# Performance work log

Hardware: AMD Instinct MI355X
Metric: run time of the kernel (lower is better)

The kernel has to match this reference:

```python
import jax, jax.numpy as jnp
import numpy as np

B, S, D = 1, 4096, 512
H, DK, DV = 8, 64, 64


def setup_inputs() -> dict:
    key = jax.random.key(0)
    ks = jax.random.split(key, 8)
    s = 1.0 / np.sqrt(D)
    return {
        "queries": jax.random.normal(ks[0], (B, S, D), jnp.float32),
        "keys": jax.random.normal(ks[1], (B, S, D), jnp.float32),
        "values": jax.random.normal(ks[2], (B, S, D), jnp.float32),
        # Linear weights stored as [in, out] for x @ W
        "Wq": jax.random.normal(ks[3], (D, H * DK), jnp.float32) * s,
        "Wk": jax.random.normal(ks[4], (D, H * DK), jnp.float32) * s,
        "Wv": jax.random.normal(ks[5], (D, H * DV), jnp.float32) * s,
        "Wo": jax.random.normal(ks[6], (H * DV, D), jnp.float32) * s,
        "bo": jax.random.normal(ks[7], (D,), jnp.float32) * 0.02,
    }


def reference(queries, keys, values, Wq, Wk, Wv, Wo, bo):
    b, qlen = values.shape[0], queries.shape[1]
    q = (queries @ Wq).reshape(b, qlen, H, DK)
    k = (keys @ Wk).reshape(b, keys.shape[1], H, DK)
    v = (values @ Wv).reshape(b, values.shape[1], H, DV)
    scale = DK ** 0.5
    # naive full attention: materialize [b, h, sq, sk] scores
    scores = jnp.einsum("bqhd,bkhd->bhqk", q, k) / scale
    attn = jax.nn.softmax(scores, axis=-1)
    out = jnp.einsum("bhqk,bkhd->bqhd", attn, v).reshape(b, qlen, H * DV)
    out = out @ Wo + bo          # first fc_out
    out = out @ Wo + bo          # second fc_out (module applies it twice when not reversible)
    return out
```

## Files before the change

### kernel.cpp

```cpp
#include <hip/hip_runtime.h>

#define S_LEN  4096
#define DMODEL 512
#define NH     8
#define HD     64

typedef _Float16 f16x8 __attribute__((ext_vector_type(8)));
typedef _Float16 f16x4 __attribute__((ext_vector_type(4)));
typedef float    f32x4 __attribute__((ext_vector_type(4)));

static __device__ __forceinline__ unsigned short f2h(float x) {
  return __builtin_bit_cast(unsigned short, (_Float16)x);
}

__global__ __launch_bounds__(256) void wtrans_kernel(
    const float* __restrict__ w0, const float* __restrict__ w1,
    const float* __restrict__ w2, const float* __restrict__ w3,
    unsigned short* __restrict__ o0, unsigned short* __restrict__ o1,
    unsigned short* __restrict__ o2, unsigned short* __restrict__ o3,
    unsigned short* __restrict__ o3s)
{
  __shared__ unsigned short T[64 * 72];
  const float* W; unsigned short* O;
  switch (blockIdx.z) {
    case 0:  W = w0; O = o0; break;
    case 1:  W = w1; O = o1; break;
    case 2:  W = w2; O = o2; break;
    default: W = w3; O = o3; break;
  }
  const int tid = threadIdx.x;
  const int k0 = blockIdx.x * 64, n0 = blockIdx.y * 64;
  const int c4 = (tid & 15) * 4;
#pragma unroll
  for (int rp = 0; rp < 4; ++rp) {
    int r = rp * 16 + (tid >> 4);
    float4 x = *(const float4*)(W + (k0 + r) * DMODEL + n0 + c4);
    T[(c4 + 0) * 72 + r] = f2h(x.x);
    T[(c4 + 1) * 72 + r] = f2h(x.y);
    T[(c4 + 2) * 72 + r] = f2h(x.z);
    T[(c4 + 3) * 72 + r] = f2h(x.w);
    if (blockIdx.z == 3) {
      f16x4 st;
      st[0] = (_Float16)x.x; st[1] = (_Float16)x.y;
      st[2] = (_Float16)x.z; st[3] = (_Float16)x.w;
      *(f16x4*)&o3s[(k0 + r) * DMODEL + n0 + c4] = st;
    }
  }
  __syncthreads();
#pragma unroll
  for (int it = 0; it < 2; ++it) {
    int i = tid + it * 256;
    int nl = i >> 3, c = i & 7;
    *(f16x8*)&O[(n0 + nl) * DMODEL + k0 + c * 8] = *(const f16x8*)&T[nl * 72 + c * 8];
  }
}

__global__ __launch_bounds__(256) void gemm128_kernel(
    const void* __restrict__ A0, const void* __restrict__ A1,
    const void* __restrict__ A2, const void* __restrict__ A3,
    const unsigned short* __restrict__ B0, const unsigned short* __restrict__ B1,
    const unsigned short* __restrict__ B2, const unsigned short* __restrict__ B3,
    void* __restrict__ C0, void* __restrict__ C1,
    void* __restrict__ C2, void* __restrict__ C3,
    const float* __restrict__ bias, unsigned short* __restrict__ vtg,
    const float* __restrict__ wo_f32, const float* __restrict__ bo_in,
    float* __restrict__ bo2_out,
    int a_fp32_mask, int c_fp32_mask)
{
  constexpr int K = DMODEL, N = DMODEL;
  __shared__ unsigned short As[128 * 32];
  __shared__ unsigned short Bs[128 * 32];
  const int z = blockIdx.z;
  if (z == 3 && blockIdx.x >= 4) {
    if (blockIdx.x < 12 && blockIdx.y == 0 && wo_f32) {
      int col = (blockIdx.x - 4) * 64 + (threadIdx.x & 63);
      float s = bo_in[col];
#pragma unroll 8
      for (int j = 0; j < DMODEL; ++j) s = fmaf(bo_in[j], wo_f32[j * DMODEL + col], s);
      bo2_out[col] = s;
    }
    return;
  }
  const void* Av; const unsigned short* Bt; void* Cv;
  switch (z) {
    case 0:  Av = A0; Bt = B0; Cv = C0; break;
    case 1:  Av = A1; Bt = B1; Cv = C1; break;
    case 2:  Av = A2; Bt = B2; Cv = C2; break;
    default: Av = A3; Bt = B3; Cv = C3; break;
  }
  const int a_fp32 = (a_fp32_mask >> z) & 1;
  const int c_fp32 = (c_fp32_mask >> z) & 1;
  const int tid  = threadIdx.x;
  const int lane = tid & 63;
  const int wid  = tid >> 6;
  const int quad = lane >> 4, l16 = lane & 15;
  const int m0 = blockIdx.x * 128, n0 = blockIdx.y * 128;
  const int wm = (wid >> 1) * 64, wn = (wid & 1) * 64;
  f32x4 acc[4][4] = {};

  f16x8 areg[2], breg[2];
#pragma unroll
  for (int it = 0; it < 2; ++it) {
    int s = it * 256 + tid;
    int r = s >> 2, ck = (s & 3) * 8;
    if (a_fp32) {
      const float* p = (const float*)Av + (m0 + r) * K + ck;
      float4 x = *(const float4*)p;
      float4 y = *(const float4*)(p + 4);
      f16x8 av;
      av[0] = (_Float16)x.x; av[1] = (_Float16)x.y;
      av[2] = (_Float16)x.z; av[3] = (_Float16)x.w;
      av[4] = (_Float16)y.x; av[5] = (_Float16)y.y;
      av[6] = (_Float16)y.z; av[7] = (_Float16)y.w;
      areg[it] = av;
    } else {
      areg[it] = *(const f16x8*)((const unsigned short*)Av + (m0 + r) * K + ck);
    }
    breg[it] = *(const f16x8*)(Bt + (n0 + r) * K + ck);
  }

  for (int k0 = 0; k0 < K; k0 += 32) {
    __syncthreads();
#pragma unroll
    for (int it = 0; it < 2; ++it) {
      int s = it * 256 + tid;
      int r = s >> 2, ck = (s & 3) * 8;
      *(f16x8*)&As[r * 32 + ck] = areg[it];
      *(f16x8*)&Bs[r * 32 + ck] = breg[it];
    }
    __syncthreads();

    if (k0 + 32 < K) {
      int kk = k0 + 32;
#pragma unroll
      for (int it = 0; it < 2; ++it) {
        int s = it * 256 + tid;
        int r = s >> 2, ck = (s & 3) * 8;
        if (a_fp32) {
          const float* p = (const float*)Av + (m0 + r) * K + kk + ck;
          float4 x = *(const float4*)p;
          float4 y = *(const float4*)(p + 4);
          f16x8 av;
          av[0] = (_Float16)x.x; av[1] = (_Float16)x.y;
          av[2] = (_Float16)x.z; av[3] = (_Float16)x.w;
          av[4] = (_Float16)y.x; av[5] = (_Float16)y.y;
          av[6] = (_Float16)y.z; av[7] = (_Float16)y.w;
          areg[it] = av;
        } else {
          areg[it] = *(const f16x8*)((const unsigned short*)Av + (m0 + r) * K + kk + ck);
        }
        breg[it] = *(const f16x8*)(Bt + (n0 + r) * K + kk + ck);
      }
    }

    f16x8 af[4], bf[4];
#pragma unroll
    for (int mt = 0; mt < 4; ++mt)
      af[mt] = *(const f16x8*)&As[(wm + mt * 16 + l16) * 32 + quad * 8];
#pragma unroll
    for (int nt = 0; nt < 4; ++nt)
      bf[nt] = *(const f16x8*)&Bs[(wn + nt * 16 + l16) * 32 + quad * 8];
#pragma unroll
    for (int mt = 0; mt < 4; ++mt)
#pragma unroll
      for (int nt = 0; nt < 4; ++nt)
        acc[mt][nt] = __builtin_amdgcn_mfma_f32_16x16x32_f16(af[mt], bf[nt], acc[mt][nt], 0, 0, 0);
  }

  const int do_vt = (vtg != nullptr) && (z == 2);
#pragma unroll
  for (int mt = 0; mt < 4; ++mt)
#pragma unroll
    for (int nt = 0; nt < 4; ++nt) {
      int col = n0 + wn + nt * 16 + l16;
      float bv = bias ? bias[col] : 0.f;
#pragma unroll
      for (int g = 0; g < 4; ++g) {
        int row = m0 + wm + mt * 16 + quad * 4 + g;
        float val = acc[mt][nt][g] + bv;
        if (do_vt)        vtg[col * S_LEN + row] = f2h(val);
        else if (c_fp32)  ((float*)Cv)[row * N + col] = val;
        else              ((unsigned short*)Cv)[row * N + col] = f2h(val);
      }
    }
}

__global__ __launch_bounds__(256) void attn_kernel(
    const unsigned short* __restrict__ Qb, const unsigned short* __restrict__ Kb,
    const unsigned short* __restrict__ VtG,
    float* __restrict__ P0, unsigned short* __restrict__ P1,
    float* __restrict__ mp, float* __restrict__ lp)
{
  __shared__ unsigned short Ks[2][64 * 72];
  __shared__ unsigned short Vt[2 * 64 * 64];
  __shared__ float Msc[2][2][16];
  __shared__ float Lsc[2][2][16];

  const int tid  = threadIdx.x;
  const int lane = tid & 63;
  const int wid  = tid >> 6;
  const int qp   = wid & 1;
  const int kh   = wid >> 1;
  const int quad = lane >> 4, l16 = lane & 15;
  const int qb = blockIdx.x, h = blockIdx.y, z = blockIdx.z;
  const int hc = h * HD;
  const int qbase = qb * 64 + qp * 32;
  const int kz = z * 2048;

  f16x8 bq[2][2];
#pragma unroll
  for (int s = 0; s < 2; ++s) {
    int qrow = qbase + s * 16 + l16;
    bq[s][0] = *(const f16x8*)(Qb + qrow * DMODEL + hc + quad * 8);
    bq[s][1] = *(const f16x8*)(Qb + qrow * DMODEL + hc + 32 + quad * 8);
  }

  f32x4 o[2][4] = {};
  float m_run[2] = {-1e30f, -1e30f}, l_run[2] = {0.f, 0.f};

  f16x8 kreg[4], vreg[4];
#pragma unroll
  for (int it = 0; it < 4; ++it) {
    int s = it * 256 + tid;
    int khs = s >> 9, n = (s >> 3) & 63, c = s & 7;
    kreg[it] = *(const f16x8*)(Kb + (kz + khs * 1024 + n) * DMODEL + hc + c * 8);
    vreg[it] = *(const f16x8*)(VtG + (hc + n) * S_LEN + kz + khs * 1024 + c * 8);
  }

  for (int kbi = 0; kbi < 16; ++kbi) {
    __syncthreads();
#pragma unroll
    for (int it = 0; it < 4; ++it) {
      int s = it * 256 + tid;
      int khs = s >> 9, n = (s >> 3) & 63, c = s & 7;
      *(f16x8*)&Ks[khs][n * 72 + c * 8] = kreg[it];
      int vbase = (khs * 64 + n) * 16;
      int n15 = n & 15;
      f16x4 lo = __builtin_shufflevector(vreg[it], vreg[it], 0, 1, 2, 3);
      f16x4 hi = __builtin_shufflevector(vreg[it], vreg[it], 4, 5, 6, 7);
      *(f16x4*)&Vt[(vbase + ((2 * c) ^ n15)) * 4]     = lo;
      *(f16x4*)&Vt[(vbase + ((2 * c + 1) ^ n15)) * 4] = hi;
    }
    __syncthreads();

    if (kbi + 1 < 16) {
      int kb1 = (kbi + 1) * 64;
#pragma unroll
      for (int it = 0; it < 4; ++it) {
        int s = it * 256 + tid;
        int khs = s >> 9, n = (s >> 3) & 63, c = s & 7;
        kreg[it] = *(const f16x8*)(Kb + (kz + khs * 1024 + kb1 + n) * DMODEL + hc + c * 8);
        vreg[it] = *(const f16x8*)(VtG + (hc + n) * S_LEN + kz + khs * 1024 + kb1 + c * 8);
      }
    }

    f32x4 sT[2][4];
#pragma unroll
    for (int kt = 0; kt < 4; ++kt) {
      f16x8 ak0 = *(const f16x8*)&Ks[kh][(kt * 16 + l16) * 72 + quad * 8];
      f16x8 ak1 = *(const f16x8*)&Ks[kh][(kt * 16 + l16) * 72 + 32 + quad * 8];
#pragma unroll
      for (int s = 0; s < 2; ++s) {
        f32x4 a = {};
        a = __builtin_amdgcn_mfma_f32_16x16x32_f16(ak0, bq[s][0], a, 0, 0, 0);
        a = __builtin_amdgcn_mfma_f32_16x16x32_f16(ak1, bq[s][1], a, 0, 0, 0);
        sT[s][kt] = a;
      }
    }

    f16x4 pa[2][4];
#pragma unroll
    for (int s = 0; s < 2; ++s) {
      float vmax = -1e30f;
#pragma unroll
      for (int kt = 0; kt < 4; ++kt)
#pragma unroll
        for (int g = 0; g < 4; ++g) vmax = fmaxf(vmax, sT[s][kt][g]);
      vmax = fmaxf(vmax, __shfl_xor(vmax, 16));
      vmax = fmaxf(vmax, __shfl_xor(vmax, 32));

      if (__all(vmax <= m_run[s] + 8.0f)) {
        const float mn = m_run[s];
        float rs = 0.f;
#pragma unroll
        for (int kt = 0; kt < 4; ++kt)
#pragma unroll
          for (int g = 0; g < 4; ++g) {
            float p = __expf((sT[s][kt][g] - mn) * 0.125f);
            rs += p;
            pa[s][kt][g] = (_Float16)p;
          }
        rs += __shfl_xor(rs, 16);
        rs += __shfl_xor(rs, 32);
        l_run[s] += rs;
      } else {
        const float mn = fmaxf(m_run[s], vmax);
        const float alpha = __expf((m_run[s] - mn) * 0.125f);
        m_run[s] = mn;

        float rs = 0.f;
#pragma unroll
        for (int kt = 0; kt < 4; ++kt)
#pragma unroll
          for (int g = 0; g < 4; ++g) {
            float p = __expf((sT[s][kt][g] - mn) * 0.125f);
            rs += p;
            pa[s][kt][g] = (_Float16)p;
          }
        rs += __shfl_xor(rs, 16);
        rs += __shfl_xor(rs, 32);
        l_run[s] = l_run[s] * alpha + rs;

        float ag[4];
#pragma unroll
        for (int g = 0; g < 4; ++g) ag[g] = __shfl(alpha, quad * 4 + g);
#pragma unroll
        for (int nt = 0; nt < 4; ++nt)
#pragma unroll
          for (int g = 0; g < 4; ++g) o[s][nt][g] *= ag[g];
      }
    }

#pragma unroll
    for (int nt = 0; nt < 4; ++nt) {
      int dbase = (kh * 64 + nt * 16 + l16) * 16;
#pragma unroll
      for (int kt = 0; kt < 4; ++kt) {
        f16x4 bv = *(const f16x4*)&Vt[(dbase + ((kt * 4 + quad) ^ l16)) * 4];
#pragma unroll
        for (int s = 0; s < 2; ++s)
          o[s][nt] = __builtin_amdgcn_mfma_f32_16x16x16f16(pa[s][kt], bv, o[s][nt], 0, 0, 0);
      }
    }
  }

  __syncthreads();
  _Float16* Osc = (_Float16*)&Ks[0][0];
  if (kh == 1) {
#pragma unroll
    for (int s = 0; s < 2; ++s) {
      if (quad == 0) { Msc[qp][s][l16] = m_run[s]; Lsc[qp][s][l16] = l_run[s]; }
#pragma unroll
      for (int nt = 0; nt < 4; ++nt)
#pragma unroll
        for (int g = 0; g < 4; ++g)
          Osc[(qp * 64 + lane) * 32 + s * 16 + nt * 4 + g] = (_Float16)o[s][nt][g];
    }
  }
  __syncthreads();
  if (kh == 0) {
#pragma unroll
    for (int s = 0; s < 2; ++s) {
      const float m1 = Msc[qp][s][l16];
      const float l1 = Lsc[qp][s][l16];
      const float m  = fmaxf(m_run[s], m1);
      const float a0 = __expf((m_run[s] - m) * 0.125f);
      const float a1 = __expf((m1 - m) * 0.125f);
      const float lt = l_run[s] * a0 + l1 * a1;
      const float rl = 1.f / lt;
      if (quad == 0) {
        int q = qbase + s * 16 + l16;
        mp[(z * NH + h) * S_LEN + q] = m;
        lp[(z * NH + h) * S_LEN + q] = lt;
      }
      float a0g[4], a1g[4], rlg[4];
#pragma unroll
      for (int g = 0; g < 4; ++g) {
        a0g[g] = __shfl(a0, quad * 4 + g);
        a1g[g] = __shfl(a1, quad * 4 + g);
        rlg[g] = __shfl(rl, quad * 4 + g);
      }
#pragma unroll
      for (int g = 0; g < 4; ++g) {
        int row = qbase + s * 16 + quad * 4 + g;
#pragma unroll
        for (int nt = 0; nt < 4; ++nt) {
          float om = o[s][nt][g] * a0g[g] + (float)Osc[(qp * 64 + lane) * 32 + s * 16 + nt * 4 + g] * a1g[g];
          float val = om * rlg[g];
          if (z == 0) P0[row * DMODEL + hc + nt * 16 + l16] = val;
          else        P1[row * DMODEL + hc + nt * 16 + l16] = f2h(val);
        }
      }
    }
  }
}

__global__ __launch_bounds__(256) void merge_kernel(
    const float* __restrict__ P0, const unsigned short* __restrict__ P1,
    const float* __restrict__ mp, const float* __restrict__ lp,
    unsigned short* __restrict__ Ob)
{
  const int tid = threadIdx.x;
  const int qb = blockIdx.x, h = blockIdx.y;
  const int q = qb * 64 + (tid >> 2), hc = h * HD;
  const int dq = (tid & 3) * 16;
  const float m0 = mp[h * S_LEN + q],        l0 = lp[h * S_LEN + q];
  const float m1 = mp[(NH + h) * S_LEN + q], l1 = lp[(NH + h) * S_LEN + q];
  const float M  = fmaxf(m0, m1);
  float w0 = l0 * __expf((m0 - M) * 0.125f);
  float w1 = l1 * __expf((m1 - M) * 0.125f);
  const float rw = 1.f / (w0 + w1);
  w0 *= rw; w1 *= rw;
  const int base = q * DMODEL + hc + dq;
  f16x8 p1a = *(const f16x8*)&P1[base];
  f16x8 p1b = *(const f16x8*)&P1[base + 8];
  float4 x0 = *(const float4*)&P0[base];
  float4 x1 = *(const float4*)&P0[base + 4];
  float4 x2 = *(const float4*)&P0[base + 8];
  float4 x3 = *(const float4*)&P0[base + 12];
  f16x8 oa, ob;
  oa[0] = (_Float16)(w0 * x0.x + w1 * (float)p1a[0]);
  oa[1] = (_Float16)(w0 * x0.y + w1 * (float)p1a[1]);
  oa[2] = (_Float16)(w0 * x0.z + w1 * (float)p1a[2]);
  oa[3] = (_Float16)(w0 * x0.w + w1 * (float)p1a[3]);
  oa[4] = (_Float16)(w0 * x1.x + w1 * (float)p1a[4]);
  oa[5] = (_Float16)(w0 * x1.y + w1 * (float)p1a[5]);
  oa[6] = (_Float16)(w0 * x1.z + w1 * (float)p1a[6]);
  oa[7] = (_Float16)(w0 * x1.w + w1 * (float)p1a[7]);
  ob[0] = (_Float16)(w0 * x2.x + w1 * (float)p1b[0]);
  ob[1] = (_Float16)(w0 * x2.y + w1 * (float)p1b[1]);
  ob[2] = (_Float16)(w0 * x2.z + w1 * (float)p1b[2]);
  ob[3] = (_Float16)(w0 * x2.w + w1 * (float)p1b[3]);
  ob[4] = (_Float16)(w0 * x3.x + w1 * (float)p1b[4]);
  ob[5] = (_Float16)(w0 * x3.y + w1 * (float)p1b[5]);
  ob[6] = (_Float16)(w0 * x3.z + w1 * (float)p1b[6]);
  ob[7] = (_Float16)(w0 * x3.w + w1 * (float)p1b[7]);
  *(f16x8*)&Ob[base]     = oa;
  *(f16x8*)&Ob[base + 8] = ob;
}

extern "C" void kernel_launch(void* const* d_in, const int* in_sizes, int n_in,
                              void* d_out, int out_size, void* d_ws, size_t ws_size,
                              hipStream_t stream) {
  const float* q  = (const float*)d_in[0];
  const float* k  = (const float*)d_in[1];
  const float* v  = (const float*)d_in[2];
  const float* Wq = (const float*)d_in[3];
  const float* Wk = (const float*)d_in[4];
  const float* Wv = (const float*)d_in[5];
  const float* Wo = (const float*)d_in[6];
  const float* bo = (const float*)d_in[7];

  unsigned short* ws   = (unsigned short*)d_ws;
  unsigned short* Wqt  = ws;
  unsigned short* Wkt  = Wqt  + 262144;
  unsigned short* Wvt  = Wkt  + 262144;
  unsigned short* Wot  = Wvt  + 262144;
  unsigned short* Wof  = Wot  + 262144;
  unsigned short* Wo2t = Wof  + 262144;
  unsigned short* Qb   = Wo2t + 262144;
  unsigned short* Kb   = Qb   + 2097152;
  unsigned short* VtG  = Kb   + 2097152;
  unsigned short* Ab   = VtG  + 2097152;
  float*          bo2  = (float*)(Ab + 2097152);
  float*          mp   = bo2 + 512;
  float*          lp   = mp + 65536;

  wtrans_kernel<<<dim3(8, 8, 4), 256, 0, stream>>>(
      Wq, Wk, Wv, Wo, Wqt, Wkt, Wvt, Wot, Wof);

  gemm128_kernel<<<dim3(32, 4, 4), 256, 0, stream>>>(
      q, k, v, Wot, Wqt, Wkt, Wvt, Wof, Qb, Kb, nullptr, Wo2t,
      nullptr, VtG, Wo, bo, bo2, 0x7, 0x0);

  attn_kernel<<<dim3(64, 8, 2), 256, 0, stream>>>(
      Qb, Kb, VtG, (float*)d_out, Ab, mp, lp);

  merge_kernel<<<dim3(64, 8), 256, 0, stream>>>(
      (const float*)d_out, Ab, mp, lp, Ab);

  gemm128_kernel<<<dim3(32, 4, 1), 256, 0, stream>>>(
      Ab, nullptr, nullptr, nullptr, Wo2t, nullptr, nullptr, nullptr,
      d_out, nullptr, nullptr, nullptr, bo2, nullptr,
      nullptr, nullptr, nullptr, 0x0, 0x1);
}
```

Baseline: 212.9 us.

## Pre-convert activations to fp16 and load GEMM tiles via global_load_lds

The fp32 to fp16 conversion of the query, key and value activations moves out of the projection GEMM into extra blocks of the weight-transpose kernel, which write fp16 copies into scratch space inside d_out and Ab. The GEMM then always reads fp16 and stages its A/B tiles straight into LDS with global_load_lds, replacing the register-prefetch software pipeline. This avoids converting inside the GEMM and cuts register use, at the cost of an extra read/write pass over the activations. Loads are no longer overlapped with MFMA work inside a block, since load and compute are now separated only by barriers.

After: 222.6 us. +4.5%, slower.

```diff
diff --git a/kernel.cpp b/kernel.cpp
--- a/kernel.cpp
+++ b/kernel.cpp
@@ -11,6 +11,12 @@
 
 static __device__ __forceinline__ unsigned short f2h(float x) {
   return __builtin_bit_cast(unsigned short, (_Float16)x);
+}
+
+static __device__ __forceinline__ void glds16(const void* g, void* l) {
+  __builtin_amdgcn_global_load_lds(
+      (const __attribute__((address_space(1))) void*)g,
+      (__attribute__((address_space(3))) void*)l, 16, 0, 0);
 }
 
 __global__ __launch_bounds__(256) void wtrans_kernel(
@@ -18,8 +24,35 @@
     const float* __restrict__ w2, const float* __restrict__ w3,
     unsigned short* __restrict__ o0, unsigned short* __restrict__ o1,
     unsigned short* __restrict__ o2, unsigned short* __restrict__ o3,
-    unsigned short* __restrict__ o3s)
+    unsigned short* __restrict__ o3s,
+    const float* __restrict__ x0, const float* __restrict__ x1,
+    const float* __restrict__ x2,
+    unsigned short* __restrict__ e0, unsigned short* __restrict__ e1,
+    unsigned short* __restrict__ e2)
 {
+  if (blockIdx.z >= 4) {
+    const float* X; unsigned short* E;
+    switch (blockIdx.z) {
+      case 4:  X = x0; E = e0; break;
+      case 5:  X = x1; E = e1; break;
+      default: X = x2; E = e2; break;
+    }
+    const int blk = blockIdx.x * 8 + blockIdx.y;
+    const int base = blk * 32768 + threadIdx.x * 8;
+#pragma unroll
+    for (int i = 0; i < 16; ++i) {
+      int off = base + i * 2048;
+      float4 a = *(const float4*)(X + off);
+      float4 b = *(const float4*)(X + off + 4);
+      f16x8 h;
+      h[0] = (_Float16)a.x; h[1] = (_Float16)a.y;
+      h[2] = (_Float16)a.z; h[3] = (_Float16)a.w;
+      h[4] = (_Float16)b.x; h[5] = (_Float16)b.y;
+      h[6] = (_Float16)b.z; h[7] = (_Float16)b.w;
+      *(f16x8*)(E + off) = h;
+    }
+    return;
+  }
   __shared__ unsigned short T[64 * 72];
   const float* W; unsigned short* O;
   switch (blockIdx.z) {
@@ -56,8 +89,8 @@
 }
 
 __global__ __launch_bounds__(256) void gemm128_kernel(
-    const void* __restrict__ A0, const void* __restrict__ A1,
-    const void* __restrict__ A2, const void* __restrict__ A3,
+    const unsigned short* __restrict__ A0, const unsigned short* __restrict__ A1,
+    const unsigned short* __restrict__ A2, const unsigned short* __restrict__ A3,
     const unsigned short* __restrict__ B0, const unsigned short* __restrict__ B1,
     const unsigned short* __restrict__ B2, const unsigned short* __restrict__ B3,
     void* __restrict__ C0, void* __restrict__ C1,
@@ -65,7 +98,7 @@
     const float* __restrict__ bias, unsigned short* __restrict__ vtg,
     const float* __restrict__ wo_f32, const float* __restrict__ bo_in,
     float* __restrict__ bo2_out,
-    int a_fp32_mask, int c_fp32_mask)
+    int c_fp32_mask)
 {
   constexpr int K = DMODEL, N = DMODEL;
   __shared__ unsigned short As[128 * 32];
@@ -81,14 +114,13 @@
     }
     return;
   }
-  const void* Av; const unsigned short* Bt; void* Cv;
+  const unsigned short* Av; const unsigned short* Bt; void* Cv;
   switch (z) {
     case 0:  Av = A0; Bt = B0; Cv = C0; break;
     case 1:  Av = A1; Bt = B1; Cv = C1; break;
     case 2:  Av = A2; Bt = B2; Cv = C2; break;
     default: Av = A3; Bt = B3; Cv = C3; break;
   }
-  const int a_fp32 = (a_fp32_mask >> z) & 1;
   const int c_fp32 = (c_fp32_mask >> z) & 1;
   const int tid  = threadIdx.x;
   const int lane = tid & 63;
@@ -98,60 +130,16 @@
   const int wm = (wid >> 1) * 64, wn = (wid & 1) * 64;
   f32x4 acc[4][4] = {};
 
-  f16x8 areg[2], breg[2];
-#pragma unroll
-  for (int it = 0; it < 2; ++it) {
-    int s = it * 256 + tid;
-    int r = s >> 2, ck = (s & 3) * 8;
-    if (a_fp32) {
-      const float* p = (const float*)Av + (m0 + r) * K + ck;
-      float4 x = *(const float4*)p;
-      float4 y = *(const float4*)(p + 4);
-      f16x8 av;
-      av[0] = (_Float16)x.x; av[1] = (_Float16)x.y;
-      av[2] = (_Float16)x.z; av[3] = (_Float16)x.w;
-      av[4] = (_Float16)y.x; av[5] = (_Float16)y.y;
-      av[6] = (_Float16)y.z; av[7] = (_Float16)y.w;
-      areg[it] = av;
-    } else {
-      areg[it] = *(const f16x8*)((const unsigned short*)Av + (m0 + r) * K + ck);
-    }
-    breg[it] = *(const f16x8*)(Bt + (n0 + r) * K + ck);
-  }
-
   for (int k0 = 0; k0 < K; k0 += 32) {
     __syncthreads();
 #pragma unroll
     for (int it = 0; it < 2; ++it) {
       int s = it * 256 + tid;
       int r = s >> 2, ck = (s & 3) * 8;
-      *(f16x8*)&As[r * 32 + ck] = areg[it];
-      *(f16x8*)&Bs[r * 32 + ck] = breg[it];
+      glds16(Av + (m0 + r) * K + k0 + ck, &As[s * 8]);
+      glds16(Bt + (n0 + r) * K + k0 + ck, &Bs[s * 8]);
     }
     __syncthreads();
-
-    if (k0 + 32 < K) {
-      int kk = k0 + 32;
-#pragma unroll
-      for (int it = 0; it < 2; ++it) {
-        int s = it * 256 + tid;
-        int r = s >> 2, ck = (s & 3) * 8;
-        if (a_fp32) {
-          const float* p = (const float*)Av + (m0 + r) * K + kk + ck;
-          float4 x = *(const float4*)p;
-          float4 y = *(const float4*)(p + 4);
-          f16x8 av;
-          av[0] = (_Float16)x.x; av[1] = (_Float16)x.y;
-          av[2] = (_Float16)x.z; av[3] = (_Float16)x.w;
-          av[4] = (_Float16)y.x; av[5] = (_Float16)y.y;
-          av[6] = (_Float16)y.z; av[7] = (_Float16)y.w;
-          areg[it] = av;
-        } else {
-          areg[it] = *(const f16x8*)((const unsigned short*)Av + (m0 + r) * K + kk + ck);
-        }
-        breg[it] = *(const f16x8*)(Bt + (n0 + r) * K + kk + ck);
-      }
-    }
 
     f16x8 af[4], bf[4];
 #pragma unroll
@@ -455,13 +443,16 @@
   float*          bo2  = (float*)(Ab + 2097152);
   float*          mp   = bo2 + 512;
   float*          lp   = mp + 65536;
-
-  wtrans_kernel<<<dim3(8, 8, 4), 256, 0, stream>>>(
-      Wq, Wk, Wv, Wo, Wqt, Wkt, Wvt, Wot, Wof);
+  unsigned short* Xq = (unsigned short*)d_out;
+  unsigned short* Xk = Xq + 2097152;
+  unsigned short* Xv = Ab;
+
+  wtrans_kernel<<<dim3(8, 8, 7), 256, 0, stream>>>(
+      Wq, Wk, Wv, Wo, Wqt, Wkt, Wvt, Wot, Wof, q, k, v, Xq, Xk, Xv);
 
   gemm128_kernel<<<dim3(32, 4, 4), 256, 0, stream>>>(
-      q, k, v, Wot, Wqt, Wkt, Wvt, Wof, Qb, Kb, nullptr, Wo2t,
-      nullptr, VtG, Wo, bo, bo2, 0x7, 0x0);
+      Xq, Xk, Xv, Wot, Wqt, Wkt, Wvt, Wof, Qb, Kb, nullptr, Wo2t,
+      nullptr, VtG, Wo, bo, bo2, 0x0);
 
   attn_kernel<<<dim3(64, 8, 2), 256, 0, stream>>>(
       Qb, Kb, VtG, (float*)d_out, Ab, mp, lp);
@@ -472,5 +463,5 @@
   gemm128_kernel<<<dim3(32, 4, 1), 256, 0, stream>>>(
       Ab, nullptr, nullptr, nullptr, Wo2t, nullptr, nullptr, nullptr,
       d_out, nullptr, nullptr, nullptr, bo2, nullptr,
-      nullptr, nullptr, nullptr, 0x0, 0x1);
-}
+      nullptr, nullptr, nullptr, 0x1);
+}
```

## Drop intra-block key split in attention; give each wave its own query rows

Applied to the files above, without the earlier changes.

Each block previously split its key range across two wave pairs that shared 64 query rows, then combined their partial softmax state through shared memory. Now all four waves process different 32-row query slices (128 rows per block) over the full 2048-key half, sharing one K/V tile per step. This removes the in-block merge, its barriers, the fp16 rounding of the partial output, and half the shared memory, and it loads each K/V tile once for twice as many query rows. In exchange the grid is halved to 512 blocks and each block runs twice as many loop iterations, which lowers parallelism.

After: 206.6 us. 1.03x faster.

```diff
diff --git a/kernel.cpp b/kernel.cpp
--- a/kernel.cpp
+++ b/kernel.cpp
@@ -191,20 +191,16 @@
     float* __restrict__ P0, unsigned short* __restrict__ P1,
     float* __restrict__ mp, float* __restrict__ lp)
 {
-  __shared__ unsigned short Ks[2][64 * 72];
-  __shared__ unsigned short Vt[2 * 64 * 64];
-  __shared__ float Msc[2][2][16];
-  __shared__ float Lsc[2][2][16];
+  __shared__ unsigned short Ks[64 * 72];
+  __shared__ unsigned short Vt[64 * 64];
 
   const int tid  = threadIdx.x;
   const int lane = tid & 63;
   const int wid  = tid >> 6;
-  const int qp   = wid & 1;
-  const int kh   = wid >> 1;
   const int quad = lane >> 4, l16 = lane & 15;
   const int qb = blockIdx.x, h = blockIdx.y, z = blockIdx.z;
   const int hc = h * HD;
-  const int qbase = qb * 64 + qp * 32;
+  const int qbase = qb * 128 + wid * 32;
   const int kz = z * 2048;
 
   f16x8 bq[2][2];
@@ -218,23 +214,23 @@
   f32x4 o[2][4] = {};
   float m_run[2] = {-1e30f, -1e30f}, l_run[2] = {0.f, 0.f};
 
-  f16x8 kreg[4], vreg[4];
-#pragma unroll
-  for (int it = 0; it < 4; ++it) {
+  f16x8 kreg[2], vreg[2];
+#pragma unroll
+  for (int it = 0; it < 2; ++it) {
     int s = it * 256 + tid;
-    int khs = s >> 9, n = (s >> 3) & 63, c = s & 7;
-    kreg[it] = *(const f16x8*)(Kb + (kz + khs * 1024 + n) * DMODEL + hc + c * 8);
-    vreg[it] = *(const f16x8*)(VtG + (hc + n) * S_LEN + kz + khs * 1024 + c * 8);
-  }
-
-  for (int kbi = 0; kbi < 16; ++kbi) {
+    int n = s >> 3, c = s & 7;
+    kreg[it] = *(const f16x8*)(Kb + (kz + n) * DMODEL + hc + c * 8);
+    vreg[it] = *(const f16x8*)(VtG + (hc + n) * S_LEN + kz + c * 8);
+  }
+
+  for (int kbi = 0; kbi < 32; ++kbi) {
     __syncthreads();
 #pragma unroll
-    for (int it = 0; it < 4; ++it) {
+    for (int it = 0; it < 2; ++it) {
       int s = it * 256 + tid;
-      int khs = s >> 9, n = (s >> 3) & 63, c = s & 7;
-      *(f16x8*)&Ks[khs][n * 72 + c * 8] = kreg[it];
-      int vbase = (khs * 64 + n) * 16;
+      int n = s >> 3, c = s & 7;
+      *(f16x8*)&Ks[n * 72 + c * 8] = kreg[it];
+      int vbase = n * 16;
       int n15 = n & 15;
       f16x4 lo = __builtin_shufflevector(vreg[it], vreg[it], 0, 1, 2, 3);
       f16x4 hi = __builtin_shufflevector(vreg[it], vreg[it], 4, 5, 6, 7);
@@ -243,22 +239,22 @@
     }
     __syncthreads();
 
-    if (kbi + 1 < 16) {
-      int kb1 = (kbi + 1) * 64;
-#pragma unroll
-      for (int it = 0; it < 4; ++it) {
+    if (kbi + 1 < 32) {
+      int kb1 = kz + (kbi + 1) * 64;
+#pragma unroll
+      for (int it = 0; it < 2; ++it) {
         int s = it * 256 + tid;
-        int khs = s >> 9, n = (s >> 3) & 63, c = s & 7;
-        kreg[it] = *(const f16x8*)(Kb + (kz + khs * 1024 + kb1 + n) * DMODEL + hc + c * 8);
-        vreg[it] = *(const f16x8*)(VtG + (hc + n) * S_LEN + kz + khs * 1024 + kb1 + c * 8);
+        int n = s >> 3, c = s & 7;
+        kreg[it] = *(const f16x8*)(Kb + (kb1 + n) * DMODEL + hc + c * 8);
+        vreg[it] = *(const f16x8*)(VtG + (hc + n) * S_LEN + kb1 + c * 8);
       }
     }
 
     f32x4 sT[2][4];
 #pragma unroll
     for (int kt = 0; kt < 4; ++kt) {
-      f16x8 ak0 = *(const f16x8*)&Ks[kh][(kt * 16 + l16) * 72 + quad * 8];
-      f16x8 ak1 = *(const f16x8*)&Ks[kh][(kt * 16 + l16) * 72 + 32 + quad * 8];
+      f16x8 ak0 = *(const f16x8*)&Ks[(kt * 16 + l16) * 72 + quad * 8];
+      f16x8 ak1 = *(const f16x8*)&Ks[(kt * 16 + l16) * 72 + 32 + quad * 8];
 #pragma unroll
       for (int s = 0; s < 2; ++s) {
         f32x4 a = {};
@@ -323,7 +319,7 @@
 
 #pragma unroll
     for (int nt = 0; nt < 4; ++nt) {
-      int dbase = (kh * 64 + nt * 16 + l16) * 16;
+      int dbase = (nt * 16 + l16) * 16;
 #pragma unroll
       for (int kt = 0; kt < 4; ++kt) {
         f16x4 bv = *(const f16x4*)&Vt[(dbase + ((kt * 4 + quad) ^ l16)) * 4];
@@ -334,52 +330,26 @@
     }
   }
 
-  __syncthreads();
-  _Float16* Osc = (_Float16*)&Ks[0][0];
-  if (kh == 1) {
-#pragma unroll
-    for (int s = 0; s < 2; ++s) {
-      if (quad == 0) { Msc[qp][s][l16] = m_run[s]; Lsc[qp][s][l16] = l_run[s]; }
-#pragma unroll
-      for (int nt = 0; nt < 4; ++nt)
-#pragma unroll
-        for (int g = 0; g < 4; ++g)
-          Osc[(qp * 64 + lane) * 32 + s * 16 + nt * 4 + g] = (_Float16)o[s][nt][g];
-    }
-  }
-  __syncthreads();
-  if (kh == 0) {
-#pragma unroll
-    for (int s = 0; s < 2; ++s) {
-      const float m1 = Msc[qp][s][l16];
-      const float l1 = Lsc[qp][s][l16];
-      const float m  = fmaxf(m_run[s], m1);
-      const float a0 = __expf((m_run[s] - m) * 0.125f);
-      const float a1 = __expf((m1 - m) * 0.125f);
-      const float lt = l_run[s] * a0 + l1 * a1;
-      const float rl = 1.f / lt;
-      if (quad == 0) {
-        int q = qbase + s * 16 + l16;
-        mp[(z * NH + h) * S_LEN + q] = m;
-        lp[(z * NH + h) * S_LEN + q] = lt;
-      }
-      float a0g[4], a1g[4], rlg[4];
-#pragma unroll
-      for (int g = 0; g < 4; ++g) {
-        a0g[g] = __shfl(a0, quad * 4 + g);
-        a1g[g] = __shfl(a1, quad * 4 + g);
-        rlg[g] = __shfl(rl, quad * 4 + g);
-      }
-#pragma unroll
-      for (int g = 0; g < 4; ++g) {
-        int row = qbase + s * 16 + quad * 4 + g;
-#pragma unroll
-        for (int nt = 0; nt < 4; ++nt) {
-          float om = o[s][nt][g] * a0g[g] + (float)Osc[(qp * 64 + lane) * 32 + s * 16 + nt * 4 + g] * a1g[g];
-          float val = om * rlg[g];
-          if (z == 0) P0[row * DMODEL + hc + nt * 16 + l16] = val;
-          else        P1[row * DMODEL + hc + nt * 16 + l16] = f2h(val);
-        }
+#pragma unroll
+  for (int s = 0; s < 2; ++s) {
+    const float lt = l_run[s];
+    const float rl = 1.f / lt;
+    if (quad == 0) {
+      int q = qbase + s * 16 + l16;
+      mp[(z * NH + h) * S_LEN + q] = m_run[s];
+      lp[(z * NH + h) * S_LEN + q] = lt;
+    }
+    float rlg[4];
+#pragma unroll
+    for (int g = 0; g < 4; ++g) rlg[g] = __shfl(rl, quad * 4 + g);
+#pragma unroll
+    for (int g = 0; g < 4; ++g) {
+      int row = qbase + s * 16 + quad * 4 + g;
+#pragma unroll
+      for (int nt = 0; nt < 4; ++nt) {
+        float val = o[s][nt][g] * rlg[g];
+        if (z == 0) P0[row * DMODEL + hc + nt * 16 + l16] = val;
+        else        P1[row * DMODEL + hc + nt * 16 + l16] = f2h(val);
       }
     }
   }
@@ -463,7 +433,7 @@
       q, k, v, Wot, Wqt, Wkt, Wvt, Wof, Qb, Kb, nullptr, Wo2t,
       nullptr, VtG, Wo, bo, bo2, 0x7, 0x0);
 
-  attn_kernel<<<dim3(64, 8, 2), 256, 0, stream>>>(
+  attn_kernel<<<dim3(32, 8, 2), 256, 0, stream>>>(
       Qb, Kb, VtG, (float*)d_out, Ab, mp, lp);
 
   merge_kernel<<<dim3(64, 8), 256, 0, stream>>>(
```
